# Optimization experiments

Hardware: AMD Instinct MI355X
Metric: run time of the kernel (lower is better)

Reference implementation:

```python
import jax, jax.numpy as jnp
import numpy as np
from jax import lax

EPS = 1e-3  # BatchNorm1d eps from norm_fn
SPARSE_SHAPE = (41, 200, 176)  # (z, y, x)
IN_CH = 4


def _conv3d(x, w, stride, pad):
    # x: [N,C,D,H,W], w: [O,I,kd,kh,kw]
    return lax.conv_general_dilated(x, w, window_strides=stride, padding=pad,
                                    dimension_numbers=('NCDHW', 'OIDHW', 'NCDHW'))


def _bn_relu(y, bn, mask):
    # eval-mode BatchNorm1d over active voxels == per-channel affine; inactive sites
    # must stay exactly 0 in a sparse tensor, hence the final mask multiply.
    g, b, m, v = bn[0], bn[1], bn[2], bn[3]
    scale = g * lax.rsqrt(v + EPS)
    shift = b - m * scale
    y = y * scale[None, :, None, None, None] + shift[None, :, None, None, None]
    return jax.nn.relu(y) * mask


def _subm(x, mask, w, bn):
    # SubMConv3d: conv evaluated only at existing active sites; active set unchanged.
    kd, kh, kw = w.shape[2:]
    pad = [(kd // 2, kd // 2), (kh // 2, kh // 2), (kw // 2, kw // 2)]
    return _bn_relu(_conv3d(x, w, (1, 1, 1), pad), bn, mask)


def _spconv(x, mask, w, bn, stride, pad):
    # SparseConv3d: output active set = sites with >=1 active input in receptive field.
    pads = [(p, p) for p in pad]
    y = _conv3d(x, w, stride, pads)
    k = tuple(w.shape[2:])
    new_mask = lax.reduce_window(mask, 0.0, lax.max, (1, 1) + k, (1, 1) + tuple(stride),
                                 [(0, 0), (0, 0)] + pads)
    new_mask = (new_mask > 0).astype(x.dtype)
    return _bn_relu(y, bn, new_mask), new_mask


def setup_inputs() -> dict:
    key = jax.random.key(0)
    ks = jax.random.split(key, 16)
    D, H, W = SPARSE_SHAPE
    mask = (jax.random.uniform(ks[0], (1, 1, D, H, W)) < 0.02).astype(jnp.float32)
    x = jax.random.normal(ks[1], (1, IN_CH, D, H, W), jnp.float32) * mask
    specs = [(16, IN_CH, (3, 3, 3)), (16, 16, (3, 3, 3)),
             (32, 16, (3, 3, 3)), (32, 32, (3, 3, 3)), (32, 32, (3, 3, 3)),
             (64, 32, (3, 3, 3)), (64, 64, (3, 3, 3)), (64, 64, (3, 3, 3)),
             (64, 64, (3, 3, 3)), (64, 64, (3, 3, 3)), (64, 64, (3, 3, 3)),
             (128, 64, (3, 1, 1))]
    inp = {'x': x, 'mask': mask}
    for i, (co, ci, k) in enumerate(specs):
        kk = jax.random.fold_in(ks[2], i)
        fan = ci * k[0] * k[1] * k[2]
        inp['w%d' % i] = jax.random.normal(kk, (co, ci) + k, jnp.float32) / np.sqrt(fan).astype(np.float32)
        inp['bn%d' % i] = jnp.stack([
            jax.random.uniform(jax.random.fold_in(kk, 1), (co,), minval=0.5, maxval=1.5),
            jax.random.normal(jax.random.fold_in(kk, 2), (co,)) * 0.1,
            jax.random.normal(jax.random.fold_in(kk, 3), (co,)) * 0.1,
            jax.random.uniform(jax.random.fold_in(kk, 4), (co,), minval=0.5, maxval=1.5)])
    return inp


def reference(x, mask, w0, bn0, w1, bn1, w2, bn2, w3, bn3, w4, bn4, w5, bn5,
              w6, bn6, w7, bn7, w8, bn8, w9, bn9, w10, bn10, w11, bn11):
    h = _subm(x, mask, w0, bn0)                       # conv_input (subm1)
    h = _subm(h, mask, w1, bn1)                       # conv1 -> x_conv1
    h, m2 = _spconv(h, mask, w2, bn2, (2, 2, 2), (1, 1, 1))  # conv2 down
    h = _subm(h, m2, w3, bn3)
    h = _subm(h, m2, w4, bn4)                         # x_conv2
    h, m3 = _spconv(h, m2, w5, bn5, (2, 2, 2), (1, 1, 1))    # conv3 down
    h = _subm(h, m3, w6, bn6)
    h = _subm(h, m3, w7, bn7)                         # x_conv3
    h, m4 = _spconv(h, m3, w8, bn8, (2, 2, 2), (0, 1, 1))    # conv4 down
    h = _subm(h, m4, w9, bn9)
    h = _subm(h, m4, w10, bn10)                       # x_conv4
    out, _ = _spconv(h, m4, w11, bn11, (2, 1, 1), (0, 0, 0)) # conv_out
    N, C, Dd, Hh, Ww = out.shape                      # [1,128,2,25,22]
    return out.reshape(N, C * Dd, Hh, Ww)             # spatial_features [1,256,25,22]
```

## Files before the change

kernel.cpp:

```cpp
#include <hip/hip_runtime.h>

#define BS 256

constexpr int D1=41, H1=200, W1=176; constexpr int N1v=D1*H1*W1;
constexpr int D2=21, H2=100, W2=88;  constexpr int N2v=D2*H2*W2;
constexpr int D3=11, H3=50,  W3=44;  constexpr int N3v=D3*H3*W3;
constexpr int D4=5,  H4=25,  W4=22;  constexpr int N4v=D4*H4*W4;
constexpr int DOo=2, HOo=25, WOo=22;
constexpr int ROWS1=40960;

typedef __attribute__((ext_vector_type(8))) short bf16x8;
typedef __attribute__((ext_vector_type(4))) float f32x4;

__device__ __forceinline__ float bflo(unsigned int u){ return __uint_as_float(u<<16); }
__device__ __forceinline__ float bfhi(unsigned int u){ return __uint_as_float(u & 0xffff0000u); }
__device__ __forceinline__ unsigned short f2bf(float f){
  unsigned int x = __float_as_uint(f);
  x += 0x7fffu + ((x>>16)&1u);
  return (unsigned short)(x>>16);
}
__device__ __forceinline__ void acc8(float& acc, uint4 p, const float* __restrict__ wk, int stride){
  acc = fmaf(bflo(p.x), wk[0*stride], acc);
  acc = fmaf(bfhi(p.x), wk[1*stride], acc);
  acc = fmaf(bflo(p.y), wk[2*stride], acc);
  acc = fmaf(bfhi(p.y), wk[3*stride], acc);
  acc = fmaf(bflo(p.z), wk[4*stride], acc);
  acc = fmaf(bfhi(p.z), wk[5*stride], acc);
  acc = fmaf(bflo(p.w), wk[6*stride], acc);
  acc = fmaf(bfhi(p.w), wk[7*stride], acc);
}

struct PrepArgs {
  const float* w[12]; const float* bn[12];
  void* dst[12]; float* bias[12];
  int O[12], I[12], K[12], mode[12];
  int off[13];
};
__global__ void prep_all(PrepArgs a){
  int t = blockIdx.x*BS + threadIdx.x;
  if (t >= a.off[12]) return;
  int li = 0;
  while (t >= a.off[li+1]) li++;
  int e = t - a.off[li];
  int O=a.O[li], I=a.I[li], K=a.K[li], mode=a.mode[li];
  const float* w = a.w[li]; const float* bn = a.bn[li];
  if (mode == 2){
    int p = e/(O*32); int rem = e - p*(O*32); int o = rem>>5; int kk = rem&31;
    int tap = 2*p + (kk>=16 ? 1 : 0); int ci = kk&15;
    float g=bn[o], b=bn[O+o], m=bn[2*O+o], v=bn[3*O+o];
    float sc = g*rsqrtf(v+1e-3f);
    float val = (tap < 27) ? w[(o*I+ci)*K + tap]*sc : 0.f;
    ((unsigned short*)a.dst[li])[e] = f2bf(val);
    if (p==0 && kk==0) a.bias[li][o] = b - m*sc;
  } else if (mode == 3){
    int ci = e % I; int tmp = e / I; int dx = tmp % 3; tmp /= 3; int o = tmp % O; int g9 = tmp / O;
    float g=bn[o], b=bn[O+o], m=bn[2*O+o], v=bn[3*O+o];
    float sc = g*rsqrtf(v+1e-3f);
    int tap = g9*3 + dx;
    ((unsigned short*)a.dst[li])[e] = f2bf(w[(o*I+ci)*27 + tap]*sc);
    if (g9==0 && dx==0 && ci==0) a.bias[li][o] = b - m*sc;
  } else {
    int k = e % K; int rest = e / K; int ci = rest % I; int o = rest / I;
    float g=bn[o], b=bn[O+o], m=bn[2*O+o], v=bn[3*O+o];
    float sc = g*rsqrtf(v+1e-3f);
    ((float*)a.dst[li])[(k*I+ci)*O + o] = w[(o*I+ci)*K + k]*sc;
    if (ci==0 && k==0) a.bias[li][o] = b - m*sc;
  }
}

__global__ void build_list1_kernel(const float* __restrict__ mask,
                                   int* __restrict__ I1, int* __restrict__ list1,
                                   int* __restrict__ cnt){
  constexpr int PER = 16;
  __shared__ int sc[BS]; __shared__ int sbase;
  int b = blockIdx.x, t = threadIdx.x;
  int base_s = b*BS*PER;
  unsigned int bits = 0; int c = 0;
  #pragma unroll
  for (int i=0;i<PER;i++){
    int s = base_s + i*BS + t;
    bool act = (s < N1v) && (mask[s] > 0.f);
    bits |= (act?1u:0u) << i; c += act;
  }
  sc[t] = c;
  __syncthreads();
  for (int ofs=1; ofs<BS; ofs<<=1){
    int v = (t>=ofs) ? sc[t-ofs] : 0;
    __syncthreads();
    sc[t] += v;
    __syncthreads();
  }
  if (t == BS-1) sbase = atomicAdd(cnt, sc[t]);
  __syncthreads();
  int pos = sbase + sc[t] - c;
  #pragma unroll
  for (int i=0;i<PER;i++){
    if (bits & (1u<<i)){
      int s = base_s + i*BS + t;
      list1[pos] = s; I1[s] = pos+1; pos++;
    }
  }
}

template<int DI,int HI,int WI,int DOUT,int HOUT,int WOUT,int PZ,int PY,int PX>
__global__ void scatter_mask_kernel(const int* __restrict__ list, const int* __restrict__ cnt, int cidx,
                                    float* __restrict__ mout){
  int t = blockIdx.x*BS + threadIdx.x;
  if (t >= cnt[cidx]) return;
  int s = list[t];
  int zz = s/(HI*WI); int rem = s - zz*(HI*WI); int yy = rem/WI; int xx = rem - yy*WI;
  int az = zz + PZ, ay = yy + PY, ax = xx + PX;
  int zlo = (az-2) <= 0 ? 0 : (az-1)/2;  int zhi = min(DOUT-1, az/2);
  int ylo = (ay-2) <= 0 ? 0 : (ay-1)/2;  int yhi = min(HOUT-1, ay/2);
  int xlo = (ax-2) <= 0 ? 0 : (ax-1)/2;  int xhi = min(WOUT-1, ax/2);
  for (int zo=zlo; zo<=zhi; zo++)
    for (int yo=ylo; yo<=yhi; yo++)
      for (int xo=xlo; xo<=xhi; xo++)
        mout[(zo*HOUT+yo)*WOUT+xo] = 1.f;
}

template<int N>
__global__ void compact_mask_kernel(const float* __restrict__ mout,
                                    int* __restrict__ list, int* __restrict__ cnt1){
  __shared__ int sc[BS]; __shared__ int sbase;
  int b = blockIdx.x, t = threadIdx.x;
  int s = b*BS + t;
  bool act = (s < N) && (mout[s] > 0.f);
  int c = act ? 1 : 0;
  sc[t] = c;
  __syncthreads();
  for (int ofs=1; ofs<BS; ofs<<=1){
    int v = (t>=ofs) ? sc[t-ofs] : 0;
    __syncthreads();
    sc[t] += v;
    __syncthreads();
  }
  if (t == BS-1) sbase = atomicAdd(cnt1, sc[t]);
  __syncthreads();
  if (act) list[sbase + sc[t] - 1] = s;
}

__global__ void subm_l0_kernel(const float* __restrict__ x,
                               const int* __restrict__ list1, const int* __restrict__ cnt,
                               const float* __restrict__ wt, const float* __restrict__ bias,
                               unsigned short* __restrict__ fout){
  __shared__ float Wl[27*4*16];
  __shared__ float Bl[16];
  int t = threadIdx.x;
  for (int e=t; e<27*4*16; e+=BS) Wl[e] = wt[e];
  if (t < 16) Bl[t] = bias[t];
  __syncthreads();
  int row = blockIdx.x*BS + t;
  if (row >= cnt[0]) return;
  int s = list1[row];
  int z = s/(H1*W1); int r = s - z*(H1*W1); int y = r/W1; int xx = r - y*W1;
  float acc[16];
  #pragma unroll
  for (int o=0;o<16;o++) acc[o] = Bl[o];
  for (int dz=-1; dz<=1; dz++){ int zz=z+dz; if ((unsigned)zz >= (unsigned)D1) continue;
    for (int dy=-1; dy<=1; dy++){ int yy=y+dy; if ((unsigned)yy >= (unsigned)H1) continue;
      for (int dx=-1; dx<=1; dx++){ int xc=xx+dx; if ((unsigned)xc >= (unsigned)W1) continue;
        int ns = (zz*H1+yy)*W1+xc;
        int k = ((dz+1)*3+(dy+1))*3+(dx+1);
        float x0 = x[ns], x1 = x[N1v+ns], x2 = x[2*N1v+ns], x3 = x[3*N1v+ns];
        const float* wk = Wl + k*64;
        #pragma unroll
        for (int o=0;o<16;o++)
          acc[o] = fmaf(x0, wk[o], fmaf(x1, wk[16+o], fmaf(x2, wk[32+o], fmaf(x3, wk[48+o], acc[o]))));
      }}}
  #pragma unroll
  for (int o=0;o<16;o++) fout[row*16+o] = f2bf(fmaxf(acc[o], 0.f));
}

template<int COUT,int HO,int WO,int PZ,int PY,int PX,int STR,bool DENSE_OUT>
__global__ __launch_bounds__(256)
void conv_mfma_l1_kernel(const unsigned short* __restrict__ fin,
                         const int* __restrict__ I1,
                         const int* __restrict__ list, const int* __restrict__ cnt, int cidx,
                         const unsigned short* __restrict__ wbt,
                         const float* __restrict__ bias,
                         unsigned short* __restrict__ outp){
  constexpr int BP = 40;
  constexpr int NT = COUT/16;
  __shared__ __align__(16) unsigned short B[14*COUT*BP];

  int nrows = cnt[cidx];
  int row0 = blockIdx.x*64;
  if (row0 >= nrows) return;

  int t = threadIdx.x;
  int lane = t & 63, wave = t >> 6;
  int m = lane & 15, quad = lane >> 4;

  constexpr int TOT = 14*COUT*32;
  for (int e = t*8; e < TOT; e += BS*8){
    int n = e >> 5, c = e & 31;
    *(uint4*)(&B[n*BP + c]) = *(const uint4*)(wbt + e);
  }

  int row = row0 + wave*16 + m;
  bool rv = row < nrows;
  int z=0, y=0, x=0;
  {
    int s = list[rv ? row : row0];
    z = s/(HO*WO); int rem = s - z*(HO*WO); y = rem/WO; x = rem - y*WO;
  }

  int rr[14];
  #pragma unroll
  for (int p=0;p<14;p++){
    int tap = 2*p + (quad>>1);
    rr[p] = 0;
    if (rv && tap < 27){
      int dz = tap/9, rem = tap - dz*9, dy = rem/3, dx = rem - dy*3;
      int zz = STR*z - PZ + dz, yy = STR*y - PY + dy, xx = STR*x - PX + dx;
      if ((unsigned)zz < (unsigned)D1 && (unsigned)yy < (unsigned)H1 && (unsigned)xx < (unsigned)W1)
        rr[p] = I1[(zz*H1+yy)*W1+xx];
    }
  }
  __syncthreads();

  f32x4 acc[NT];
  #pragma unroll
  for (int i=0;i<NT;i++) acc[i] = (f32x4){0.f,0.f,0.f,0.f};

  bf16x8 acur = (bf16x8){0,0,0,0,0,0,0,0};
  if (rr[0] > 0) acur = *(const bf16x8*)(fin + (size_t)(rr[0]-1)*16 + (quad&1)*8);
  #pragma unroll
  for (int p=0;p<14;p++){
    bf16x8 anext = (bf16x8){0,0,0,0,0,0,0,0};
    if (p < 13 && rr[p+1] > 0)
      anext = *(const bf16x8*)(fin + (size_t)(rr[p+1]-1)*16 + (quad&1)*8);
    #pragma unroll
    for (int nt=0; nt<NT; nt++){
      bf16x8 b = *(const bf16x8*)(&B[(p*COUT + nt*16 + m)*BP + quad*8]);
      acc[nt] = __builtin_amdgcn_mfma_f32_16x16x32_bf16(acur, b, acc[nt], 0, 0, 0);
    }
    acur = anext;
  }

  #pragma unroll
  for (int nt=0; nt<NT; nt++){
    int cout = nt*16 + m;
    float bv = bias[cout];
    #pragma unroll
    for (int rg=0; rg<4; rg++){
      int rw = row0 + wave*16 + quad*4 + rg;
      if (rw < nrows){
        float v = fmaxf(acc[nt][rg] + bv, 0.f);
        if (DENSE_OUT){
          int s = list[rw];
          outp[(size_t)s*COUT + cout] = f2bf(v);
        } else {
          outp[(size_t)rw*COUT + cout] = f2bf(v);
        }
      }
    }
  }
}

template<int CIN,int COUT,int DI,int HI,int WI,int HO,int WO,int PZ,int PY,int PX,int STR>
__global__ __launch_bounds__(256)
void conv_mfma2_kernel(const unsigned short* __restrict__ gin,
                       const int* __restrict__ list, const int* __restrict__ cnt, int cidx,
                       const unsigned short* __restrict__ wg,
                       const float* __restrict__ bias,
                       unsigned short* __restrict__ gout){
  constexpr int KW = 3*CIN;
  constexpr int BP = KW + 8;
  constexpr int NT = COUT/16;
  constexpr int KT = KW/32;
  constexpr int PREN = (COUT*KW + BS*8 - 1)/(BS*8);
  __shared__ __align__(16) unsigned short B[2][COUT*BP];

  int nrows = cnt[cidx];
  int row0 = blockIdx.x*64;
  if (row0 >= nrows) return;

  int t = threadIdx.x;
  int lane = t & 63, wave = t >> 6;
  int m = lane & 15, quad = lane >> 4;

  #pragma unroll
  for (int i=0;i<PREN;i++){
    int e = t*8 + i*BS*8;
    if (e < COUT*KW){
      int n = e / KW, c = e - n*KW;
      *(uint4*)(&B[0][n*BP + c]) = *(const uint4*)(wg + e);
    }
  }

  int row = row0 + wave*16 + m;
  bool rv = row < nrows;
  int z=0, y=0, x=0;
  {
    int s = list[rv ? row : row0];
    z = s/(HO*WO); int rem = s - z*(HO*WO); y = rem/WO; x = rem - y*WO;
  }

  auto loadA = [&](int g, bf16x8* av){
    int dz = g/3, dy = g - dz*3;
    int zz = STR*z - PZ + dz, yy = STR*y - PY + dy, xx0 = STR*x - PX;
    bool zyok = rv && (unsigned)zz < (unsigned)DI && (unsigned)yy < (unsigned)HI;
    int base = ((zz*HI + yy)*WI + xx0)*CIN;
    #pragma unroll
    for (int kt=0; kt<KT; kt++){
      int tapx = (kt*32)/CIN;
      av[kt] = (bf16x8){0,0,0,0,0,0,0,0};
      if (zyok && (unsigned)(xx0 + tapx) < (unsigned)WI)
        av[kt] = *(const bf16x8*)(gin + (size_t)(base + kt*32 + quad*8));
    }
  };

  f32x4 acc[NT];
  #pragma unroll
  for (int i=0;i<NT;i++) acc[i] = (f32x4){0.f,0.f,0.f,0.f};

  bf16x8 acur[KT], anext[KT];
  loadA(0, acur);
  __syncthreads();

  #pragma unroll
  for (int g=0; g<9; g++){
    uint4 pre[PREN];
    if (g < 8){
      const unsigned short* src = wg + (size_t)(g+1)*COUT*KW;
      #pragma unroll
      for (int i=0;i<PREN;i++){
        int e = t*8 + i*BS*8;
        pre[i] = (e < COUT*KW) ? *(const uint4*)(src + e) : (uint4){0,0,0,0};
      }
      loadA(g+1, anext);
    }
    #pragma unroll
    for (int kt=0; kt<KT; kt++){
      #pragma unroll
      for (int nt=0; nt<NT; nt++){
        bf16x8 b = *(const bf16x8*)(&B[g&1][(nt*16 + m)*BP + kt*32 + quad*8]);
        acc[nt] = __builtin_amdgcn_mfma_f32_16x16x32_bf16(acur[kt], b, acc[nt], 0, 0, 0);
      }
    }
    if (g < 8){
      #pragma unroll
      for (int i=0;i<PREN;i++){
        int e = t*8 + i*BS*8;
        if (e < COUT*KW){
          int n = e / KW, c = e - n*KW;
          *(uint4*)(&B[(g+1)&1][n*BP + c]) = pre[i];
        }
      }
      #pragma unroll
      for (int kt=0; kt<KT; kt++) acur[kt] = anext[kt];
    }
    __syncthreads();
  }

  #pragma unroll
  for (int nt=0; nt<NT; nt++){
    int cout = nt*16 + m;
    float bv = bias[cout];
    #pragma unroll
    for (int rg=0; rg<4; rg++){
      int rw = row0 + wave*16 + quad*4 + rg;
      if (rw < nrows){
        int s = list[rw];
        gout[(size_t)s*COUT + cout] = f2bf(fmaxf(acc[nt][rg] + bv, 0.f));
      }
    }
  }
}

__global__ void conv_out_kernel(const unsigned short* __restrict__ g4,
                                const float* __restrict__ m4,
                                const float* __restrict__ wt, const float* __restrict__ bias,
                                float* __restrict__ out){
  int t = blockIdx.x*BS + threadIdx.x;
  if (t >= 128*DOo*HOo*WOo) return;
  int cout = t & 127; int s = t >> 7;
  int d = s/(HOo*WOo); int r = s - d*(HOo*WOo); int h = r/WOo; int w = r - h*WOo;
  float res = 0.f;
  bool act = false;
  float acc = bias[cout];
  for (int dz=0; dz<3; dz++){
    int z4 = 2*d + dz;
    int site = (z4*H4 + h)*W4 + w;
    if (m4[site] == 0.f) continue;
    act = true;
    const uint4* fr = (const uint4*)(g4 + (size_t)site*64);
    const float* wk = wt + dz*64*128 + cout;
    #pragma unroll
    for (int q=0; q<8; q++) acc8(acc, fr[q], wk + q*8*128, 128);
  }
  if (act) res = fmaxf(acc, 0.f);
  out[((cout*DOo + d)*HOo + h)*WOo + w] = res;
}

extern "C" void kernel_launch(void* const* d_in, const int* in_sizes, int n_in,
                              void* d_out, int out_size, void* d_ws, size_t ws_size,
                              hipStream_t stream){
  const float* x    = (const float*)d_in[0];
  const float* mask = (const float*)d_in[1];
  const float* w[12]; const float* bnp[12];
  for (int i=0;i<12;i++){ w[i]=(const float*)d_in[2+2*i]; bnp[i]=(const float*)d_in[3+2*i]; }

  char* base = (char*)d_ws; size_t off = 0;
  auto alloc = [&](size_t b)->void*{ void* p = base + off; off = (off + b + 255) & ~(size_t)255; return p; };

  int* cnt   = (int*)alloc(16);
  int* I1    = (int*)alloc((size_t)N1v*4);
  unsigned short* g2a = (unsigned short*)alloc((size_t)N2v*32*2);
  unsigned short* g2b = (unsigned short*)alloc((size_t)N2v*32*2);
  unsigned short* g3a = (unsigned short*)alloc((size_t)N3v*64*2);
  unsigned short* g3b = (unsigned short*)alloc((size_t)N3v*64*2);
  unsigned short* g4a = (unsigned short*)alloc((size_t)N4v*64*2);
  unsigned short* g4b = (unsigned short*)alloc((size_t)N4v*64*2);
  float* m2 = (float*)alloc((size_t)N2v*4);
  float* m3 = (float*)alloc((size_t)N3v*4);
  float* m4 = (float*)alloc((size_t)N4v*4);
  size_t zero_bytes = off;
  int* list1 = (int*)alloc((size_t)ROWS1*4);
  unsigned short* f1a = (unsigned short*)alloc((size_t)ROWS1*16*2);
  unsigned short* f1b = (unsigned short*)alloc((size_t)ROWS1*16*2);
  int* list2 = (int*)alloc((size_t)N2v*4);
  int* list3 = (int*)alloc((size_t)N3v*4);
  int* list4 = (int*)alloc((size_t)N4v*4);

  static const int Oa[12]={16,16,32,32,32,64,64,64,64,64,64,128};
  static const int Ia[12]={ 4,16,16,32,32,32,64,64,64,64,64, 64};
  static const int Ka[12]={27,27,27,27,27,27,27,27,27,27,27,  3};
  static const int Ma[12]={ 0, 2, 2, 3, 3, 3, 3, 3, 3, 3, 3,  0};
  float* wt[12]; float* bs[12]; unsigned short* wbt[12];
  for (int i=0;i<12;i++){
    bs[i] = (float*)alloc((size_t)Oa[i]*4);
    wt[i]=nullptr; wbt[i]=nullptr;
    if (Ma[i]==0)      wt[i]  = (float*)alloc((size_t)Oa[i]*Ia[i]*Ka[i]*4);
    else if (Ma[i]==3) wbt[i] = (unsigned short*)alloc((size_t)Oa[i]*Ia[i]*27*2);
    else               wbt[i] = (unsigned short*)alloc((size_t)14*Oa[i]*32*2);
  }

  hipMemsetAsync(base, 0, zero_bytes, stream);

  PrepArgs pa;
  pa.off[0] = 0;
  for (int i=0;i<12;i++){
    pa.w[i]=w[i]; pa.bn[i]=bnp[i]; pa.bias[i]=bs[i];
    pa.O[i]=Oa[i]; pa.I[i]=Ia[i]; pa.K[i]=Ka[i]; pa.mode[i]=Ma[i];
    pa.dst[i] = (Ma[i]==0) ? (void*)wt[i] : (void*)wbt[i];
    int tot = (Ma[i]==2) ? 14*Oa[i]*32 : Oa[i]*Ia[i]*Ka[i];
    pa.off[i+1] = pa.off[i] + tot;
  }
  prep_all<<<(pa.off[12]+BS-1)/BS, BS, 0, stream>>>(pa);

  build_list1_kernel<<<(N1v + BS*16 - 1)/(BS*16), BS, 0, stream>>>(mask, I1, list1, cnt);

  subm_l0_kernel<<<(ROWS1+BS-1)/BS, BS, 0, stream>>>(x, list1, cnt, wt[0], bs[0], f1a);
  conv_mfma_l1_kernel<16,H1,W1,1,1,1,1,false><<<ROWS1/64, 256, 0, stream>>>
      (f1a, I1, list1, cnt, 0, wbt[1], bs[1], f1b);

  scatter_mask_kernel<D1,H1,W1,D2,H2,W2,1,1,1><<<(ROWS1+BS-1)/BS, BS, 0, stream>>>(list1, cnt, 0, m2);
  compact_mask_kernel<N2v><<<(N2v+BS-1)/BS, BS, 0, stream>>>(m2, list2, cnt+1);
  conv_mfma_l1_kernel<32,H2,W2,1,1,1,2,true><<<(N2v+63)/64, 256, 0, stream>>>
      (f1b, I1, list2, cnt, 1, wbt[2], bs[2], g2a);

  {
    int nb = (N2v + 63)/64;
    conv_mfma2_kernel<32,32,D2,H2,W2,H2,W2,1,1,1,1><<<nb, 256, 0, stream>>>(g2a, list2, cnt, 1, wbt[3], bs[3], g2b);
    conv_mfma2_kernel<32,32,D2,H2,W2,H2,W2,1,1,1,1><<<nb, 256, 0, stream>>>(g2b, list2, cnt, 1, wbt[4], bs[4], g2a);
  }

  scatter_mask_kernel<D2,H2,W2,D3,H3,W3,1,1,1><<<(N2v+BS-1)/BS, BS, 0, stream>>>(list2, cnt, 1, m3);
  compact_mask_kernel<N3v><<<(N3v+BS-1)/BS, BS, 0, stream>>>(m3, list3, cnt+2);
  {
    int nb = (N3v + 63)/64;
    conv_mfma2_kernel<32,64,D2,H2,W2,H3,W3,1,1,1,2><<<nb, 256, 0, stream>>>(g2a, list3, cnt, 2, wbt[5], bs[5], g3a);
    conv_mfma2_kernel<64,64,D3,H3,W3,H3,W3,1,1,1,1><<<nb, 256, 0, stream>>>(g3a, list3, cnt, 2, wbt[6], bs[6], g3b);
    conv_mfma2_kernel<64,64,D3,H3,W3,H3,W3,1,1,1,1><<<nb, 256, 0, stream>>>(g3b, list3, cnt, 2, wbt[7], bs[7], g3a);
  }

  scatter_mask_kernel<D3,H3,W3,D4,H4,W4,0,1,1><<<(N3v+BS-1)/BS, BS, 0, stream>>>(list3, cnt, 2, m4);
  compact_mask_kernel<N4v><<<(N4v+BS-1)/BS, BS, 0, stream>>>(m4, list4, cnt+3);
  {
    int nb = (N4v + 63)/64;
    conv_mfma2_kernel<64,64,D3,H3,W3,H4,W4,0,1,1,2><<<nb, 256, 0, stream>>>(g3a, list4, cnt, 3, wbt[8], bs[8], g4a);
    conv_mfma2_kernel<64,64,D4,H4,W4,H4,W4,1,1,1,1><<<nb, 256, 0, stream>>>(g4a, list4, cnt, 3, wbt[9], bs[9], g4b);
    conv_mfma2_kernel<64,64,D4,H4,W4,H4,W4,1,1,1,1><<<nb, 256, 0, stream>>>(g4b, list4, cnt, 3, wbt[10], bs[10], g4a);
  }

  conv_out_kernel<<<(128*DOo*HOo*WOo)/BS, BS, 0, stream>>>(g4a, m4, wt[11], bs[11], (float*)d_out);
}
```

Measured before the change: 403.3 us.

## Add tap-split MFMA conv kernel for small layers and channel-last bf16 input

Introduces conv_tp_kernel, which processes 16 output rows per block and splits the nine (dz,dy) tap groups across four waves, then reduces the partial sums through shared memory. It replaces the 64-row conv_mfma2 launches for the conv3 downsample and all conv4-stage layers, giving these small layers more blocks to fill the GPU at the cost of an extra shared-memory reduction and weights read straight from global memory. Separately, build_list1 now also writes the 4-channel input as channel-last bf16, so subm_l0 does one 8-byte load per tap instead of four strided fp32 loads, and its tap loops are fully unrolled. The conversion reads the whole dense input, adds a full-grid write, and rounds the input to bf16.

```diff
diff --git a/kernel.cpp b/kernel.cpp
--- a/kernel.cpp
+++ b/kernel.cpp
@@ -69,6 +69,8 @@
 }
 
 __global__ void build_list1_kernel(const float* __restrict__ mask,
+                                   const float* __restrict__ x,
+                                   unsigned short* __restrict__ xcl,
                                    int* __restrict__ I1, int* __restrict__ list1,
                                    int* __restrict__ cnt){
   constexpr int PER = 16;
@@ -79,7 +81,14 @@
   #pragma unroll
   for (int i=0;i<PER;i++){
     int s = base_s + i*BS + t;
-    bool act = (s < N1v) && (mask[s] > 0.f);
+    bool act = false;
+    if (s < N1v){
+      act = mask[s] > 0.f;
+      unsigned short h0 = f2bf(x[s]),       h1 = f2bf(x[N1v+s]);
+      unsigned short h2 = f2bf(x[2*N1v+s]), h3 = f2bf(x[3*N1v+s]);
+      uint2 pk; pk.x = ((unsigned)h1<<16)|h0; pk.y = ((unsigned)h3<<16)|h2;
+      *(uint2*)(xcl + (size_t)s*4) = pk;
+    }
     bits |= (act?1u:0u) << i; c += act;
   }
   sc[t] = c;
@@ -140,7 +149,7 @@
   if (act) list[sbase + sc[t] - 1] = s;
 }
 
-__global__ void subm_l0_kernel(const float* __restrict__ x,
+__global__ void subm_l0_kernel(const unsigned short* __restrict__ xcl,
                                const int* __restrict__ list1, const int* __restrict__ cnt,
                                const float* __restrict__ wt, const float* __restrict__ bias,
                                unsigned short* __restrict__ fout){
@@ -157,12 +166,16 @@
   float acc[16];
   #pragma unroll
   for (int o=0;o<16;o++) acc[o] = Bl[o];
+  #pragma unroll
   for (int dz=-1; dz<=1; dz++){ int zz=z+dz; if ((unsigned)zz >= (unsigned)D1) continue;
+    #pragma unroll
     for (int dy=-1; dy<=1; dy++){ int yy=y+dy; if ((unsigned)yy >= (unsigned)H1) continue;
+      #pragma unroll
       for (int dx=-1; dx<=1; dx++){ int xc=xx+dx; if ((unsigned)xc >= (unsigned)W1) continue;
         int ns = (zz*H1+yy)*W1+xc;
         int k = ((dz+1)*3+(dy+1))*3+(dx+1);
-        float x0 = x[ns], x1 = x[N1v+ns], x2 = x[2*N1v+ns], x3 = x[3*N1v+ns];
+        uint2 pk = *(const uint2*)(xcl + (size_t)ns*4);
+        float x0 = bflo(pk.x), x1 = bfhi(pk.x), x2 = bflo(pk.y), x3 = bfhi(pk.y);
         const float* wk = Wl + k*64;
         #pragma unroll
         for (int o=0;o<16;o++)
@@ -366,6 +379,94 @@
         int s = list[rw];
         gout[(size_t)s*COUT + cout] = f2bf(fmaxf(acc[nt][rg] + bv, 0.f));
       }
+    }
+  }
+}
+
+template<int CIN,int COUT,int DI,int HI,int WI,int HO,int WO,int PZ,int PY,int PX,int STR>
+__global__ __launch_bounds__(256)
+void conv_tp_kernel(const unsigned short* __restrict__ gin,
+                    const int* __restrict__ list, const int* __restrict__ cnt, int cidx,
+                    const unsigned short* __restrict__ wg,
+                    const float* __restrict__ bias,
+                    unsigned short* __restrict__ gout){
+  constexpr int KW = 3*CIN;
+  constexpr int NT = COUT/16;
+  constexpr int KT = KW/32;
+  __shared__ float R[4][NT*256];
+
+  int nrows = cnt[cidx];
+  int row0 = blockIdx.x*16;
+  if (row0 >= nrows) return;
+
+  int t = threadIdx.x;
+  int lane = t & 63, wave = t >> 6;
+  int m = lane & 15, quad = lane >> 4;
+
+  int row = row0 + m;
+  bool rv = row < nrows;
+  int z=0, y=0, x=0;
+  {
+    int s = list[rv ? row : row0];
+    z = s/(HO*WO); int rem = s - z*(HO*WO); y = rem/WO; x = rem - y*WO;
+  }
+
+  bf16x8 av[3][KT];
+  #pragma unroll
+  for (int i=0;i<3;i++){
+    int g = wave + i*4;
+    #pragma unroll
+    for (int kt=0; kt<KT; kt++) av[i][kt] = (bf16x8){0,0,0,0,0,0,0,0};
+    if (g < 9){
+      int dz = g/3, dy = g - dz*3;
+      int zz = STR*z - PZ + dz, yy = STR*y - PY + dy, xx0 = STR*x - PX;
+      bool zyok = rv && (unsigned)zz < (unsigned)DI && (unsigned)yy < (unsigned)HI;
+      int base = ((zz*HI + yy)*WI + xx0)*CIN;
+      #pragma unroll
+      for (int kt=0; kt<KT; kt++){
+        int tapx = (kt*32)/CIN;
+        if (zyok && (unsigned)(xx0 + tapx) < (unsigned)WI)
+          av[i][kt] = *(const bf16x8*)(gin + (size_t)(base + kt*32 + quad*8));
+      }
+    }
+  }
+
+  f32x4 acc[NT];
+  #pragma unroll
+  for (int i=0;i<NT;i++) acc[i] = (f32x4){0.f,0.f,0.f,0.f};
+
+  #pragma unroll
+  for (int i=0;i<3;i++){
+    int g = wave + i*4;
+    if (g < 9){
+      const unsigned short* wsrc = wg + (size_t)g*COUT*KW;
+      #pragma unroll
+      for (int kt=0; kt<KT; kt++){
+        #pragma unroll
+        for (int nt=0; nt<NT; nt++){
+          bf16x8 b = *(const bf16x8*)(wsrc + (size_t)(nt*16 + m)*KW + kt*32 + quad*8);
+          acc[nt] = __builtin_amdgcn_mfma_f32_16x16x32_bf16(av[i][kt], b, acc[nt], 0, 0, 0);
+        }
+      }
+    }
+  }
+
+  #pragma unroll
+  for (int nt=0; nt<NT; nt++)
+    #pragma unroll
+    for (int rg=0; rg<4; rg++)
+      R[wave][nt*256 + (quad*4+rg)*16 + m] = acc[nt][rg];
+  __syncthreads();
+
+  for (int e = t; e < 16*COUT; e += BS){
+    int r = e / COUT, cout = e % COUT;
+    int nt = cout >> 4, mm = cout & 15;
+    int idx = nt*256 + r*16 + mm;
+    float sum = R[0][idx] + R[1][idx] + R[2][idx] + R[3][idx];
+    int rw = row0 + r;
+    if (rw < nrows){
+      int s = list[rw];
+      gout[(size_t)s*COUT + cout] = f2bf(fmaxf(sum + bias[cout], 0.f));
     }
   }
 }
@@ -418,6 +519,7 @@
   float* m3 = (float*)alloc((size_t)N3v*4);
   float* m4 = (float*)alloc((size_t)N4v*4);
   size_t zero_bytes = off;
+  unsigned short* xcl = (unsigned short*)alloc((size_t)N1v*4*2);
   int* list1 = (int*)alloc((size_t)ROWS1*4);
   unsigned short* f1a = (unsigned short*)alloc((size_t)ROWS1*16*2);
   unsigned short* f1b = (unsigned short*)alloc((size_t)ROWS1*16*2);
@@ -451,9 +553,9 @@
   }
   prep_all<<<(pa.off[12]+BS-1)/BS, BS, 0, stream>>>(pa);
 
-  build_list1_kernel<<<(N1v + BS*16 - 1)/(BS*16), BS, 0, stream>>>(mask, I1, list1, cnt);
-
-  subm_l0_kernel<<<(ROWS1+BS-1)/BS, BS, 0, stream>>>(x, list1, cnt, wt[0], bs[0], f1a);
+  build_list1_kernel<<<(N1v + BS*16 - 1)/(BS*16), BS, 0, stream>>>(mask, x, xcl, I1, list1, cnt);
+
+  subm_l0_kernel<<<(ROWS1+BS-1)/BS, BS, 0, stream>>>(xcl, list1, cnt, wt[0], bs[0], f1a);
   conv_mfma_l1_kernel<16,H1,W1,1,1,1,1,false><<<ROWS1/64, 256, 0, stream>>>
       (f1a, I1, list1, cnt, 0, wbt[1], bs[1], f1b);
 
@@ -471,8 +573,8 @@
   scatter_mask_kernel<D2,H2,W2,D3,H3,W3,1,1,1><<<(N2v+BS-1)/BS, BS, 0, stream>>>(list2, cnt, 1, m3);
   compact_mask_kernel<N3v><<<(N3v+BS-1)/BS, BS, 0, stream>>>(m3, list3, cnt+2);
   {
+    conv_tp_kernel<32,64,D2,H2,W2,H3,W3,1,1,1,2><<<(N3v+15)/16, 256, 0, stream>>>(g2a, list3, cnt, 2, wbt[5], bs[5], g3a);
     int nb = (N3v + 63)/64;
-    conv_mfma2_kernel<32,64,D2,H2,W2,H3,W3,1,1,1,2><<<nb, 256, 0, stream>>>(g2a, list3, cnt, 2, wbt[5], bs[5], g3a);
     conv_mfma2_kernel<64,64,D3,H3,W3,H3,W3,1,1,1,1><<<nb, 256, 0, stream>>>(g3a, list3, cnt, 2, wbt[6], bs[6], g3b);
     conv_mfma2_kernel<64,64,D3,H3,W3,H3,W3,1,1,1,1><<<nb, 256, 0, stream>>>(g3b, list3, cnt, 2, wbt[7], bs[7], g3a);
   }
@@ -480,10 +582,10 @@
   scatter_mask_kernel<D3,H3,W3,D4,H4,W4,0,1,1><<<(N3v+BS-1)/BS, BS, 0, stream>>>(list3, cnt, 2, m4);
   compact_mask_kernel<N4v><<<(N4v+BS-1)/BS, BS, 0, stream>>>(m4, list4, cnt+3);
   {
-    int nb = (N4v + 63)/64;
-    conv_mfma2_kernel<64,64,D3,H3,W3,H4,W4,0,1,1,2><<<nb, 256, 0, stream>>>(g3a, list4, cnt, 3, wbt[8], bs[8], g4a);
-    conv_mfma2_kernel<64,64,D4,H4,W4,H4,W4,1,1,1,1><<<nb, 256, 0, stream>>>(g4a, list4, cnt, 3, wbt[9], bs[9], g4b);
-    conv_mfma2_kernel<64,64,D4,H4,W4,H4,W4,1,1,1,1><<<nb, 256, 0, stream>>>(g4b, list4, cnt, 3, wbt[10], bs[10], g4a);
+    int nb = (N4v + 15)/16;
+    conv_tp_kernel<64,64,D3,H3,W3,H4,W4,0,1,1,2><<<nb, 256, 0, stream>>>(g3a, list4, cnt, 3, wbt[8], bs[8], g4a);
+    conv_tp_kernel<64,64,D4,H4,W4,H4,W4,1,1,1,1><<<nb, 256, 0, stream>>>(g4a, list4, cnt, 3, wbt[9], bs[9], g4b);
+    conv_tp_kernel<64,64,D4,H4,W4,H4,W4,1,1,1,1><<<nb, 256, 0, stream>>>(g4b, list4, cnt, 3, wbt[10], bs[10], g4a);
   }
 
   conv_out_kernel<<<(128*DOo*HOo*WOo)/BS, BS, 0, stream>>>(g4a, m4, wt[11], bs[11], (float*)d_out);
```

After: 360.9 us. -10.5%, faster.
